# Kernel tuning notes

Hardware: AMD Instinct MI355X
Metric: run time of the kernel (lower is better)

## Reference

```python
import jax, jax.numpy as jnp
import numpy as np

B, C, T, W, H, N = 8, 512, 64, 14, 14, 3
EPS = 1e-6


def setup_inputs() -> dict:
    key = jax.random.key(0)
    ks = jax.random.split(key, 7)
    video = jax.random.normal(ks[0], (B, C, T, W, H), dtype=jnp.float32)
    # per-clip length; original code uses actual video length (here = T frames)
    length = jnp.full((B,), float(T), dtype=jnp.float32)
    mu_t = 0.5 * jax.random.normal(ks[1], (N,), dtype=jnp.float32)
    mu_x = 0.5 * jax.random.normal(ks[2], (N,), dtype=jnp.float32)
    mu_y = 0.5 * jax.random.normal(ks[3], (N,), dtype=jnp.float32)
    sigma_t = 1e-4 * jax.random.normal(ks[4], (N,), dtype=jnp.float32)
    sigma_x = 1e-4 * jax.random.normal(ks[5], (N,), dtype=jnp.float32)
    sigma_y = 1e-4 * jax.random.normal(ks[6], (N,), dtype=jnp.float32)
    return {"video": video, "length": length, "mu_t": mu_t, "mu_x": mu_x,
            "mu_y": mu_y, "sigma_t": sigma_t, "sigma_x": sigma_x, "sigma_y": sigma_y}


def reference(video, length, mu_t, mu_x, mu_y, sigma_t, sigma_x, sigma_y):
    b, c, t_len, w_len, h_len = video.shape
    dt = video.dtype
    # sigma transform: scale * exp(1.5 - 2|tanh(sigma)|); covariance is diagonal,
    # so the 3x3 inverse in the original is just 1/(sigma^2 + eps) per axis.
    st = jnp.exp(1.5 - 2.0 * jnp.abs(jnp.tanh(sigma_t)))
    sx = jnp.exp(1.5 - 2.0 * jnp.abs(jnp.tanh(sigma_x)))
    sy = jnp.exp(1.5 - 2.0 * jnp.abs(jnp.tanh(sigma_y)))
    pt = 1.0 / (st * st + EPS)  # (N,) precisions
    px = 1.0 / (sx * sx + EPS)
    py = 1.0 / (sy * sy + EPS)
    # means mapped to grid coordinates
    mu_tb = (length[:, None] - 1.0) * (jnp.tanh(mu_t)[None, :] + 1.0) * 0.5  # (B,N)
    mu_xv = (w_len - 1) * (jnp.tanh(mu_x) + 1.0) * 0.5                        # (N,)
    mu_yv = (h_len - 1) * (jnp.tanh(mu_y) + 1.0) * 0.5                        # (N,)
    tg = jnp.arange(t_len, dtype=dt)
    xg = jnp.arange(w_len, dtype=dt)
    yg = jnp.arange(h_len, dtype=dt)
    # separable quadratic terms
    qt = pt[None, :, None] * (tg[None, None, :] - mu_tb[:, :, None]) ** 2  # (B,N,T)
    qx = px[:, None] * (xg[None, :] - mu_xv[:, None]) ** 2                 # (N,W)
    qy = py[:, None] * (yg[None, :] - mu_yv[:, None]) ** 2                 # (N,H)
    expo = (qt[:, :, :, None, None]
            + qx[None, :, None, :, None]
            + qy[None, :, None, None, :])                                  # (B,N,T,W,H)
    f = jnp.exp(-0.5 * expo)
    f = f / (jnp.sum(f, axis=(2, 3, 4), keepdims=True) + EPS)
    # weighted-sum pooling against the video: (B, C, N) -> (B, C*N)
    o = jnp.einsum('bnthw,bcthw->bcn', f, video)
    return o.reshape(b, c * N)
```

## Files before the change

kernel.cpp:

```cpp
#include <hip/hip_runtime.h>
#include <math.h>

#define B_ 8
#define C_ 512
#define T_ 64
#define W_ 14
#define H_ 14
#define N_ 3
#define EPSF 1e-6f
#define WH (W_*H_)
#define TWH (T_*W_*H_)
#define NF4 (TWH/4)

__global__ void TSF_weights_kernel(const float* __restrict__ length,
                                   const float* __restrict__ mu_t,
                                   const float* __restrict__ mu_x,
                                   const float* __restrict__ mu_y,
                                   const float* __restrict__ sigma_t,
                                   const float* __restrict__ sigma_x,
                                   const float* __restrict__ sigma_y,
                                   float* __restrict__ wt,
                                   float* __restrict__ wxy)
{
    __shared__ float s_wxy[N_][WH];
    __shared__ float s_ft[B_][N_][T_];
    __shared__ float s_sxy[N_];
    __shared__ float s_st[B_][N_];
    const int tid = threadIdx.x;

    for (int i = tid; i < N_*WH; i += blockDim.x) {
        int n = i / WH;
        int r = i - n*WH;
        int w = r / H_;
        int h = r - w*H_;
        float sx = expf(1.5f - 2.0f*fabsf(tanhf(sigma_x[n])));
        float sy = expf(1.5f - 2.0f*fabsf(tanhf(sigma_y[n])));
        float px = 1.0f/(sx*sx + EPSF);
        float py = 1.0f/(sy*sy + EPSF);
        float mx = (float)(W_-1) * (tanhf(mu_x[n]) + 1.0f) * 0.5f;
        float my = (float)(H_-1) * (tanhf(mu_y[n]) + 1.0f) * 0.5f;
        float dx = (float)w - mx;
        float dy = (float)h - my;
        s_wxy[n][r] = expf(-0.5f*(px*dx*dx + py*dy*dy));
    }
    for (int i = tid; i < B_*N_*T_; i += blockDim.x) {
        int b  = i / (N_*T_);
        int rm = i - b*(N_*T_);
        int n  = rm / T_;
        int t  = rm - n*T_;
        float st = expf(1.5f - 2.0f*fabsf(tanhf(sigma_t[n])));
        float pt = 1.0f/(st*st + EPSF);
        float mt = (length[b] - 1.0f) * (tanhf(mu_t[n]) + 1.0f) * 0.5f;
        float d  = (float)t - mt;
        s_ft[b][n][t] = expf(-0.5f*pt*d*d);
    }
    __syncthreads();

    if (tid < N_) {
        float s = 0.f;
        for (int r = 0; r < WH; ++r) s += s_wxy[tid][r];
        s_sxy[tid] = s;
    }
    if (tid >= 32 && tid < 32 + B_*N_) {
        int i = tid - 32;
        int b = i / N_, n = i - b*N_;
        float s = 0.f;
        for (int t = 0; t < T_; ++t) s += s_ft[b][n][t];
        s_st[b][n] = s;
    }
    __syncthreads();

    for (int i = tid; i < N_*WH; i += blockDim.x)
        wxy[i] = (&s_wxy[0][0])[i];
    for (int i = tid; i < B_*N_*T_; i += blockDim.x) {
        int b  = i / (N_*T_);
        int rm = i - b*(N_*T_);
        int n  = rm / T_;
        float Z = s_st[b][n] * s_sxy[n];
        wt[i] = (&s_ft[0][0][0])[i] * (1.0f/(Z + EPSF));
    }
}

__global__ __launch_bounds__(256) void TSF_pool_kernel(
        const float* __restrict__ video,
        const float* __restrict__ wt,
        const float* __restrict__ wxy,
        float* __restrict__ out)
{
    const int bc = blockIdx.x;
    const int b  = bc >> 9;
    const int tid = threadIdx.x;

    __shared__ float s_wt[N_][T_];
    __shared__ float s_wxy[N_][WH];
    for (int i = tid; i < N_*T_;  i += 256) (&s_wt[0][0])[i]  = wt[b*N_*T_ + i];
    for (int i = tid; i < N_*WH; i += 256) (&s_wxy[0][0])[i] = wxy[i];
    __syncthreads();

    const float4* vp = (const float4*)(video + (size_t)bc * TWH);
    float a0 = 0.f, a1 = 0.f, a2 = 0.f;
    for (int p = tid; p < NF4; p += 256) {
        float4 v = vp[p];
        int e = p << 2;
        int t = e / WH;
        int r = e - t*WH;
        float4 w0 = *(const float4*)&s_wxy[0][r];
        float4 w1 = *(const float4*)&s_wxy[1][r];
        float4 w2 = *(const float4*)&s_wxy[2][r];
        float d0 = v.x*w0.x + v.y*w0.y + v.z*w0.z + v.w*w0.w;
        float d1 = v.x*w1.x + v.y*w1.y + v.z*w1.z + v.w*w1.w;
        float d2 = v.x*w2.x + v.y*w2.y + v.z*w2.z + v.w*w2.w;
        a0 += s_wt[0][t]*d0;
        a1 += s_wt[1][t]*d1;
        a2 += s_wt[2][t]*d2;
    }

    for (int off = 32; off > 0; off >>= 1) {
        a0 += __shfl_down(a0, off, 64);
        a1 += __shfl_down(a1, off, 64);
        a2 += __shfl_down(a2, off, 64);
    }
    __shared__ float s_red[4][N_];
    const int wave = tid >> 6;
    if ((tid & 63) == 0) {
        s_red[wave][0] = a0; s_red[wave][1] = a1; s_red[wave][2] = a2;
    }
    __syncthreads();
    if (tid < N_) {
        float s = s_red[0][tid] + s_red[1][tid] + s_red[2][tid] + s_red[3][tid];
        out[(size_t)bc * N_ + tid] = s;
    }
}

extern "C" void kernel_launch(void* const* d_in, const int* in_sizes, int n_in,
                              void* d_out, int out_size, void* d_ws, size_t ws_size,
                              hipStream_t stream) {
    const float* video   = (const float*)d_in[0];
    const float* length  = (const float*)d_in[1];
    const float* mu_t    = (const float*)d_in[2];
    const float* mu_x    = (const float*)d_in[3];
    const float* mu_y    = (const float*)d_in[4];
    const float* sigma_t = (const float*)d_in[5];
    const float* sigma_x = (const float*)d_in[6];
    const float* sigma_y = (const float*)d_in[7];

    float* wt  = (float*)d_ws;
    float* wxy = wt + B_*N_*T_;

    TSF_weights_kernel<<<1, 256, 0, stream>>>(length, mu_t, mu_x, mu_y,
                                              sigma_t, sigma_x, sigma_y, wt, wxy);
    TSF_pool_kernel<<<B_*C_, 256, 0, stream>>>(video, wt, wxy, (float*)d_out);
}
```

Before: 45.12 us.

## Fuse Gaussian weight computation into pooling kernel and drop separate launch

Removes the single-block weights kernel and has each pooling block recompute the temporal and spatial Gaussian weights and their normalisers in shared memory. Three waves each build one component, using wave-level xor shuffles for the sums. This removes a kernel launch, the serialised single-block dependency, and the workspace round trip. In exchange, every one of the 4096 blocks repeats a small amount of transcendental math before streaming the video.

New measurement: 38.35 us. -15.0%, faster.

```diff
diff --git a/kernel.cpp b/kernel.cpp
--- a/kernel.cpp
+++ b/kernel.cpp
@@ -12,89 +12,66 @@
 #define TWH (T_*W_*H_)
 #define NF4 (TWH/4)
 
-__global__ void TSF_weights_kernel(const float* __restrict__ length,
-                                   const float* __restrict__ mu_t,
-                                   const float* __restrict__ mu_x,
-                                   const float* __restrict__ mu_y,
-                                   const float* __restrict__ sigma_t,
-                                   const float* __restrict__ sigma_x,
-                                   const float* __restrict__ sigma_y,
-                                   float* __restrict__ wt,
-                                   float* __restrict__ wxy)
-{
-    __shared__ float s_wxy[N_][WH];
-    __shared__ float s_ft[B_][N_][T_];
-    __shared__ float s_sxy[N_];
-    __shared__ float s_st[B_][N_];
-    const int tid = threadIdx.x;
-
-    for (int i = tid; i < N_*WH; i += blockDim.x) {
-        int n = i / WH;
-        int r = i - n*WH;
-        int w = r / H_;
-        int h = r - w*H_;
-        float sx = expf(1.5f - 2.0f*fabsf(tanhf(sigma_x[n])));
-        float sy = expf(1.5f - 2.0f*fabsf(tanhf(sigma_y[n])));
-        float px = 1.0f/(sx*sx + EPSF);
-        float py = 1.0f/(sy*sy + EPSF);
-        float mx = (float)(W_-1) * (tanhf(mu_x[n]) + 1.0f) * 0.5f;
-        float my = (float)(H_-1) * (tanhf(mu_y[n]) + 1.0f) * 0.5f;
-        float dx = (float)w - mx;
-        float dy = (float)h - my;
-        s_wxy[n][r] = expf(-0.5f*(px*dx*dx + py*dy*dy));
-    }
-    for (int i = tid; i < B_*N_*T_; i += blockDim.x) {
-        int b  = i / (N_*T_);
-        int rm = i - b*(N_*T_);
-        int n  = rm / T_;
-        int t  = rm - n*T_;
-        float st = expf(1.5f - 2.0f*fabsf(tanhf(sigma_t[n])));
-        float pt = 1.0f/(st*st + EPSF);
-        float mt = (length[b] - 1.0f) * (tanhf(mu_t[n]) + 1.0f) * 0.5f;
-        float d  = (float)t - mt;
-        s_ft[b][n][t] = expf(-0.5f*pt*d*d);
-    }
-    __syncthreads();
-
-    if (tid < N_) {
-        float s = 0.f;
-        for (int r = 0; r < WH; ++r) s += s_wxy[tid][r];
-        s_sxy[tid] = s;
-    }
-    if (tid >= 32 && tid < 32 + B_*N_) {
-        int i = tid - 32;
-        int b = i / N_, n = i - b*N_;
-        float s = 0.f;
-        for (int t = 0; t < T_; ++t) s += s_ft[b][n][t];
-        s_st[b][n] = s;
-    }
-    __syncthreads();
-
-    for (int i = tid; i < N_*WH; i += blockDim.x)
-        wxy[i] = (&s_wxy[0][0])[i];
-    for (int i = tid; i < B_*N_*T_; i += blockDim.x) {
-        int b  = i / (N_*T_);
-        int rm = i - b*(N_*T_);
-        int n  = rm / T_;
-        float Z = s_st[b][n] * s_sxy[n];
-        wt[i] = (&s_ft[0][0][0])[i] * (1.0f/(Z + EPSF));
-    }
-}
-
-__global__ __launch_bounds__(256) void TSF_pool_kernel(
+__global__ __launch_bounds__(256) void TSF_fused_kernel(
         const float* __restrict__ video,
-        const float* __restrict__ wt,
-        const float* __restrict__ wxy,
+        const float* __restrict__ length,
+        const float* __restrict__ mu_t,
+        const float* __restrict__ mu_x,
+        const float* __restrict__ mu_y,
+        const float* __restrict__ sigma_t,
+        const float* __restrict__ sigma_x,
+        const float* __restrict__ sigma_y,
         float* __restrict__ out)
 {
-    const int bc = blockIdx.x;
-    const int b  = bc >> 9;
+    const int bc  = blockIdx.x;
+    const int b   = bc >> 9;
     const int tid = threadIdx.x;
+    const int wave = tid >> 6;
+    const int lane = tid & 63;
 
     __shared__ float s_wt[N_][T_];
     __shared__ float s_wxy[N_][WH];
-    for (int i = tid; i < N_*T_;  i += 256) (&s_wt[0][0])[i]  = wt[b*N_*T_ + i];
-    for (int i = tid; i < N_*WH; i += 256) (&s_wxy[0][0])[i] = wxy[i];
+
+    if (wave < N_) {
+        const int n = wave;
+        float st = expf(1.5f - 2.0f*fabsf(tanhf(sigma_t[n])));
+        float sx = expf(1.5f - 2.0f*fabsf(tanhf(sigma_x[n])));
+        float sy = expf(1.5f - 2.0f*fabsf(tanhf(sigma_y[n])));
+        float pt = 1.0f/(st*st + EPSF);
+        float px = 1.0f/(sx*sx + EPSF);
+        float py = 1.0f/(sy*sy + EPSF);
+        float mt = (length[b] - 1.0f) * (tanhf(mu_t[n]) + 1.0f) * 0.5f;
+        float mx = (float)(W_-1) * (tanhf(mu_x[n]) + 1.0f) * 0.5f;
+        float my = (float)(H_-1) * (tanhf(mu_y[n]) + 1.0f) * 0.5f;
+
+        float dtv = (float)lane - mt;
+        float ftv = expf(-0.5f*pt*dtv*dtv);
+        float sft = ftv;
+        #pragma unroll
+        for (int off = 1; off < 64; off <<= 1)
+            sft += __shfl_xor(sft, off, 64);
+
+        float swxy = 0.f;
+        #pragma unroll
+        for (int k = 0; k < 4; ++k) {
+            int r = lane + 64*k;
+            if (r < WH) {
+                int w = r / H_;
+                int h = r - w*H_;
+                float dx = (float)w - mx;
+                float dy = (float)h - my;
+                float v = expf(-0.5f*(px*dx*dx + py*dy*dy));
+                s_wxy[n][r] = v;
+                swxy += v;
+            }
+        }
+        #pragma unroll
+        for (int off = 1; off < 64; off <<= 1)
+            swxy += __shfl_xor(swxy, off, 64);
+
+        float norm = 1.0f / (sft*swxy + EPSF);
+        s_wt[n][lane] = ftv * norm;
+    }
     __syncthreads();
 
     const float4* vp = (const float4*)(video + (size_t)bc * TWH);
@@ -115,14 +92,14 @@
         a2 += s_wt[2][t]*d2;
     }
 
+    #pragma unroll
     for (int off = 32; off > 0; off >>= 1) {
         a0 += __shfl_down(a0, off, 64);
         a1 += __shfl_down(a1, off, 64);
         a2 += __shfl_down(a2, off, 64);
     }
     __shared__ float s_red[4][N_];
-    const int wave = tid >> 6;
-    if ((tid & 63) == 0) {
+    if (lane == 0) {
         s_red[wave][0] = a0; s_red[wave][1] = a1; s_red[wave][2] = a2;
     }
     __syncthreads();
@@ -144,10 +121,7 @@
     const float* sigma_x = (const float*)d_in[6];
     const float* sigma_y = (const float*)d_in[7];
 
-    float* wt  = (float*)d_ws;
-    float* wxy = wt + B_*N_*T_;
-
-    TSF_weights_kernel<<<1, 256, 0, stream>>>(length, mu_t, mu_x, mu_y,
-                                              sigma_t, sigma_x, sigma_y, wt, wxy);
-    TSF_pool_kernel<<<B_*C_, 256, 0, stream>>>(video, wt, wxy, (float*)d_out);
+    TSF_fused_kernel<<<B_*C_, 256, 0, stream>>>(video, length, mu_t, mu_x, mu_y,
+                                                sigma_t, sigma_x, sigma_y,
+                                                (float*)d_out);
 }
```
